# Optimization experiments

Hardware: AMD Instinct MI355X
Metric: run time of the kernel (lower is better)

Reference implementation:

```python
import jax, jax.numpy as jnp
import numpy as np

SCALE = 10  # scaling_factor
ETA = 1.0   # init arg eta
EPS = 1e-20


def setup_inputs() -> dict:
    key = jax.random.key(0)
    k1, k2, k3 = jax.random.split(key, 3)
    B, H, W = 32, 1280, 1280
    h, w = H // SCALE, W // SCALE
    output = jax.random.uniform(k1, (B, 1, H, W), dtype=jnp.float32)
    target = jax.random.uniform(k2, (B, 1, H, W), dtype=jnp.float32)
    inp = jax.random.uniform(k3, (B, 1, h, w), dtype=jnp.float32)
    return {"output": output, "target": target, "inp": inp}


def _box_downsample(x):
    # scipy valid convolve2d with ones(10,10)/100 then [::10,::10] strided slice
    # == non-overlapping 10x10 average pooling (H, W divisible by 10).
    B, H, W = x.shape
    return x.reshape(B, H // SCALE, SCALE, W // SCALE, SCALE).mean(axis=(2, 4))


def reference(output, target, inp):
    # MSE term: conv output is computed from detached numpy in the original,
    # so no gradient flows through the pooling path -> stop_gradient.
    pooled = jax.lax.stop_gradient(_box_downsample(output[:, 0]))  # [B, h, w]
    mse = jnp.mean(ETA * (inp[:, 0] - pooled) ** 2)
    # BCE-style term with exact-zero replacement (matches x[x==0]=1e-20)
    om = jnp.where(output == 0, EPS, output)
    oc_raw = 1.0 - output
    oc = jnp.where(oc_raw == 0, EPS, oc_raw)
    bce = -jnp.mean(target * jnp.log(om) + (1.0 - target) * jnp.log(oc))
    loss = mse + bce
    return jnp.full((1, 1), loss)  # original returns a (1,1) tensor
```

## Files before the change

### kernel.cpp

```cpp
#include <hip/hip_runtime.h>


#define BATCH 32
#define HH 1280
#define WW 1280
#define PH 128
#define PW 128
#define SC 10
#define NT 640
#define NV ((SC * WW) / 4)
#define KITER (NV / NT)

static constexpr float EPSV = 1e-20f;
static constexpr float INV_NB = 1.0f / (float)(BATCH * HH * WW);
static constexpr float INV_NM = 1.0f / (float)(BATCH * PH * PW);

__global__ __launch_bounds__(NT) void srloss_kernel(
    const float* __restrict__ output,
    const float* __restrict__ target,
    const float* __restrict__ inp,
    float* __restrict__ out)
{
    __shared__ float psum[PW];
    __shared__ float red[NT / 64];

    const int t = threadIdx.x;
    const int band = blockIdx.x;
    const int b = band >> 7;
    const int pr = band & 127;

    if (t < PW) psum[t] = 0.0f;
    __syncthreads();

    const size_t base = ((size_t)b * HH + (size_t)pr * SC) * WW;
    const float4* __restrict__ o4p = (const float4*)(output + base);
    const float4* __restrict__ t4p = (const float4*)(target + base);

    float4 ov[KITER], tv[KITER];
    #pragma unroll
    for (int k = 0; k < KITER; ++k) ov[k] = o4p[t + NT * k];
    #pragma unroll
    for (int k = 0; k < KITER; ++k) tv[k] = t4p[t + NT * k];

    float bce_acc = 0.0f;
    float s0 = 0.0f, s1 = 0.0f;
    #pragma unroll
    for (int k = 0; k < KITER; ++k) {
        const float o[4]  = {ov[k].x, ov[k].y, ov[k].z, ov[k].w};
        const float tg[4] = {tv[k].x, tv[k].y, tv[k].z, tv[k].w};
        #pragma unroll
        for (int j = 0; j < 4; ++j) {
            const float om  = (o[j] == 0.0f) ? EPSV : o[j];
            const float ocr = 1.0f - o[j];
            const float oc  = (ocr == 0.0f) ? EPSV : ocr;
            bce_acc += tg[j] * __logf(om) + (1.0f - tg[j]) * __logf(oc);
        }
        s0 += o[0] + o[1];
        s1 += o[2] + o[3];
    }

    const int col0 = 4 * (t % 320);
    const int p0 = col0 / SC;
    if ((col0 % SC) == 8) {
        atomicAdd(&psum[p0],     s0);
        atomicAdd(&psum[p0 + 1], s1);
    } else {
        atomicAdd(&psum[p0], s0 + s1);
    }
    __syncthreads();

    float mse_acc = 0.0f;
    if (t < PW) {
        const float pooled = psum[t] * (1.0f / (float)(SC * SC));
        const float iv = inp[(size_t)band * PW + t];
        const float d = iv - pooled;
        mse_acc = d * d;
    }

    float contrib = (-INV_NB) * bce_acc + INV_NM * mse_acc;

    #pragma unroll
    for (int off = 32; off > 0; off >>= 1)
        contrib += __shfl_down(contrib, off, 64);
    if ((t & 63) == 0) red[t >> 6] = contrib;
    __syncthreads();
    if (t == 0) {
        float s = 0.0f;
        #pragma unroll
        for (int w = 0; w < NT / 64; ++w) s += red[w];
        atomicAdd(out, s);
    }
}

extern "C" void kernel_launch(void* const* d_in, const int* in_sizes, int n_in,
                              void* d_out, int out_size, void* d_ws, size_t ws_size,
                              hipStream_t stream) {
    const float* output = (const float*)d_in[0];
    const float* target = (const float*)d_in[1];
    const float* inp    = (const float*)d_in[2];
    float* out = (float*)d_out;

    hipMemsetAsync(out, 0, sizeof(float), stream);

    srloss_kernel<<<BATCH * PH, NT, 0, stream>>>(output, target, inp, out);
}
```

Before: 413.8 us.

## Halve block size, software-pipeline row loads, and simplify log math

Each block now uses 320 threads that walk the 10-row band one row at a time, with a 4-deep rotating register prefetch buffer in place of loading all data up front. It also asks for 8 blocks per CU. The BCE term now uses log2 with one fused difference term, scaled by ln2 at the end, and replaces the exact-zero checks with fmaxf clamps. The goal is lower register pressure and higher occupancy to hide memory latency, with fewer ALU ops per element. The fmaxf clamp differs from the reference only for inputs outside [0,1].

Measured after the change: 436.9 us. +5.6%, slower.

```diff
diff --git a/kernel.cpp b/kernel.cpp
--- a/kernel.cpp
+++ b/kernel.cpp
@@ -7,15 +7,16 @@
 #define PH 128
 #define PW 128
 #define SC 10
-#define NT 640
-#define NV ((SC * WW) / 4)
-#define KITER (NV / NT)
+#define NT 320
+#define KD 10
+#define PD 4
 
 static constexpr float EPSV = 1e-20f;
+static constexpr float LN2  = 0.6931471805599453f;
 static constexpr float INV_NB = 1.0f / (float)(BATCH * HH * WW);
 static constexpr float INV_NM = 1.0f / (float)(BATCH * PH * PW);
 
-__global__ __launch_bounds__(NT) void srloss_kernel(
+__global__ __launch_bounds__(NT, 8) void srloss_kernel(
     const float* __restrict__ output,
     const float* __restrict__ target,
     const float* __restrict__ inp,
@@ -33,33 +34,44 @@
     __syncthreads();
 
     const size_t base = ((size_t)b * HH + (size_t)pr * SC) * WW;
-    const float4* __restrict__ o4p = (const float4*)(output + base);
-    const float4* __restrict__ t4p = (const float4*)(target + base);
+    const float4* __restrict__ o4p = (const float4*)(output + base) + t;
+    const float4* __restrict__ t4p = (const float4*)(target + base) + t;
 
-    float4 ov[KITER], tv[KITER];
+    float4 ob[PD], tb[PD];
     #pragma unroll
-    for (int k = 0; k < KITER; ++k) ov[k] = o4p[t + NT * k];
-    #pragma unroll
-    for (int k = 0; k < KITER; ++k) tv[k] = t4p[t + NT * k];
+    for (int k = 0; k < PD; ++k) {
+        ob[k] = o4p[NT * k];
+        tb[k] = t4p[NT * k];
+    }
 
-    float bce_acc = 0.0f;
+    float acc2 = 0.0f;
+    float accd = 0.0f;
     float s0 = 0.0f, s1 = 0.0f;
     #pragma unroll
-    for (int k = 0; k < KITER; ++k) {
-        const float o[4]  = {ov[k].x, ov[k].y, ov[k].z, ov[k].w};
-        const float tg[4] = {tv[k].x, tv[k].y, tv[k].z, tv[k].w};
+    for (int k = 0; k < KD; ++k) {
+        const float4 o4 = ob[k & (PD - 1)];
+        const float4 t4 = tb[k & (PD - 1)];
+        if (k + PD < KD) {
+            ob[k & (PD - 1)] = o4p[NT * (k + PD)];
+            tb[k & (PD - 1)] = t4p[NT * (k + PD)];
+        }
+        const float o[4]  = {o4.x, o4.y, o4.z, o4.w};
+        const float tg[4] = {t4.x, t4.y, t4.z, t4.w};
         #pragma unroll
         for (int j = 0; j < 4; ++j) {
-            const float om  = (o[j] == 0.0f) ? EPSV : o[j];
-            const float ocr = 1.0f - o[j];
-            const float oc  = (ocr == 0.0f) ? EPSV : ocr;
-            bce_acc += tg[j] * __logf(om) + (1.0f - tg[j]) * __logf(oc);
+            const float om = fmaxf(o[j], EPSV);
+            const float oc = fmaxf(1.0f - o[j], EPSV);
+            const float l1 = __log2f(om);
+            const float l2 = __log2f(oc);
+            acc2 += l2;
+            accd += tg[j] * (l1 - l2);
         }
         s0 += o[0] + o[1];
         s1 += o[2] + o[3];
     }
+    const float bce_acc = LN2 * (acc2 + accd);
 
-    const int col0 = 4 * (t % 320);
+    const int col0 = 4 * t;
     const int p0 = col0 / SC;
     if ((col0 % SC) == 8) {
         atomicAdd(&psum[p0],     s0);
```
